# Performance work log

Hardware: AMD Instinct MI355X
Metric: run time of the kernel (lower is better)

The kernel has to match this reference:

```python
import jax, jax.numpy as jnp
import numpy as np

NF, NH1, NH21, NH22, NCLS = 6, 128, 128, 128, 3
OBS_X, OBS_Y, OBS_Z, R = 10.0, 10.0, 9.0, 7.0
BATCH = 131072


def setup_inputs() -> dict:
    key = jax.random.key(0)
    ks = jax.random.split(key, 16)
    def lin(kw, kb, fan_in, fan_out):
        bound = 1.0 / np.sqrt(fan_in)
        w = jax.random.uniform(kw, (fan_out, fan_in), jnp.float32, -bound, bound)
        b = jax.random.uniform(kb, (fan_out,), jnp.float32, -bound, bound)
        return w, b
    fc1_w, fc1_b = lin(ks[0], ks[1], NF, NH1)
    fc21_w, fc21_b = lin(ks[2], ks[3], NH1, NH21)
    fc22_w, fc22_b = lin(ks[4], ks[5], NH1, NH22)
    fcm1_w, fcm1_b = lin(ks[6], ks[7], NH21, NH21)
    fcm2_w, fcm2_b = lin(ks[8], ks[9], NH22, NH22)
    fc31_w, fc31_b = lin(ks[10], ks[11], NH21, NCLS)
    fc32_w, fc32_b = lin(ks[12], ks[13], NH22, 2)
    x = jax.random.normal(ks[14], (BATCH, NF), jnp.float32)
    mean = jnp.array([10.0, 0.0, 10.0, 0.0, 9.0, 0.0], jnp.float32)
    std = jnp.array([5.0, 2.0, 5.0, 2.0, 5.0, 2.0], jnp.float32)
    return {"x": x, "mean": mean, "std": std,
            "fc1_w": fc1_w, "fc1_b": fc1_b,
            "fc21_w": fc21_w, "fc21_b": fc21_b,
            "fc22_w": fc22_w, "fc22_b": fc22_b,
            "fcm1_w": fcm1_w, "fcm1_b": fcm1_b,
            "fcm2_w": fcm2_w, "fcm2_b": fcm2_b,
            "fc31_w": fc31_w, "fc31_b": fc31_b,
            "fc32_w": fc32_w, "fc32_b": fc32_b,
            "sgn": 1}


def _forward(x, mean, std, fc1_w, fc1_b, fc21_w, fc21_b, fc22_w, fc22_b,
             fcm1_w, fcm1_b, fcm2_w, fcm2_b, fc31_w, fc31_b, fc32_w, fc32_b):
    x0 = x * std + mean                                   # de-normalized state [B,6]
    h = jnp.tanh(x @ fc1_w.T + fc1_b)                     # [B,NH1]
    x21 = jnp.tanh(h @ fc21_w.T + fc21_b)
    x22 = jnp.tanh(h @ fc22_w.T + fc22_b)
    x21 = jnp.tanh(x21 @ fcm1_w.T + fcm1_b)
    x22 = jnp.tanh(x22 @ fcm2_w.T + fcm2_b)
    x31 = x21 @ fc31_w.T + fc31_b                         # QP linear term p, [B,3]
    x32 = 4.0 * jax.nn.sigmoid(x22 @ fc32_w.T + fc32_b)   # HOCBF penalties, [B,2]

    # higher-order CBF terms
    px, vx, py, vy, pz, vz = (x0[:, i] for i in range(6))
    dx, dy, dz = px - OBS_X, py - OBS_Y, pz - OBS_Z
    barrier = dx**4 + dy**4 + dz**4 - R**4
    barrier_dot = 4.0 * (dx**3 * vx + dy**3 * vy + dz**3 * vz)
    Lf2b = 12.0 * (dx**2 * vx**2 + dy**2 * vy**2 + dz**2 * vz**2)
    G = -4.0 * jnp.stack([dx**3, dy**3, dz**3], axis=-1)  # [B,3], single constraint G u <= h
    hvec = Lf2b + (x32[:, 0] + x32[:, 1]) * barrier_dot + x32[:, 0] * x32[:, 1] * barrier  # [B]

    # QP: min 0.5 u^T u + x31^T u  s.t.  G u <= h  (Q = I, one constraint)
    # Closed-form KKT: u = -x31 - lam*G, lam = max(0, (G @ (-x31) - h) / (G @ G))
    u_unc = -x31
    Gu = jnp.sum(G * u_unc, axis=-1)                      # [B]
    GG = jnp.sum(G * G, axis=-1)                          # [B]
    lam = jnp.maximum(Gu - hvec, 0.0) / GG
    u = u_unc - lam[:, None] * G                          # [B,3]
    return u


def reference(x, mean, std, fc1_w, fc1_b, fc21_w, fc21_b, fc22_w, fc22_b,
              fcm1_w, fcm1_b, fcm2_w, fcm2_b, fc31_w, fc31_b, fc32_w, fc32_b, sgn):
    return _forward(x, mean, std, fc1_w, fc1_b, fc21_w, fc21_b, fc22_w, fc22_b,
                    fcm1_w, fcm1_b, fcm2_w, fcm2_b, fc31_w, fc31_b, fc32_w, fc32_b)
```

## Files before the change

### kernel.cpp

```cpp
#include <hip/hip_runtime.h>

typedef _Float16 half8 __attribute__((ext_vector_type(8)));
typedef _Float16 half4_t __attribute__((ext_vector_type(4)));
typedef float float4_t __attribute__((ext_vector_type(4)));

#define SB 32
#define NT 256

#define OFF_W1   0
#define OFF_W21  4096
#define OFF_W22  20480
#define OFF_WM1  36864
#define OFF_WM2  53248
#define OFF_W4   69632
#define OFF_BIAS 70272
#define WS_WELEMS 70272

__device__ __forceinline__ float fast_tanh(float x) {
  float e = __builtin_amdgcn_exp2f(x * 2.8853900817779268f);
  return fmaf(-2.f, __builtin_amdgcn_rcpf(1.f + e), 1.f);
}
__device__ __forceinline__ float sigmoid4(float z) {
  float e = __builtin_amdgcn_exp2f(-z * 1.4426950408889634f);
  return 4.f * __builtin_amdgcn_rcpf(1.f + e);
}

__global__ void prepack(const float* __restrict__ w1, const float* __restrict__ w21,
                        const float* __restrict__ w22, const float* __restrict__ wm1,
                        const float* __restrict__ wm2, const float* __restrict__ w31,
                        const float* __restrict__ w32, const float* __restrict__ b1,
                        const float* __restrict__ b21, const float* __restrict__ b22,
                        const float* __restrict__ bm1, const float* __restrict__ bm2,
                        _Float16* __restrict__ ws) {
  const int stride = gridDim.x * blockDim.x;
  for (int i = blockIdx.x * blockDim.x + threadIdx.x; i < WS_WELEMS; i += stride) {
    float v;
    if (i < OFF_W21) {
      int t = i;
      int j = t & 7, c = t >> 3, l16 = c & 15, t1 = c >> 4;
      int k8 = t1 & 3, mt = t1 >> 2;
      int row = mt * 16 + l16, k = k8 * 8 + j;
      v = (k < 6) ? w1[row * 6 + k] : 0.f;
    } else if (i < OFF_W4) {
      int t = i - OFF_W21;
      int m = t >> 14; t &= 16383;
      const float* src = (m == 0) ? w21 : (m == 1) ? w22 : (m == 2) ? wm1 : wm2;
      int j = t & 7, c = t >> 3, l16 = c & 15, t1 = c >> 4;
      int k8 = t1 & 15, mt = t1 >> 4;
      v = src[(mt * 16 + l16) * 128 + k8 * 8 + j];
    } else {
      int t = i - OFF_W4;
      int r = t >> 7, k = t & 127;
      v = (r < 3) ? w31[r * 128 + k] : w32[(r - 3) * 128 + k];
    }
    ws[i] = (_Float16)v;
  }
  float* bws = (float*)(ws + OFF_BIAS);
  for (int i = blockIdx.x * blockDim.x + threadIdx.x; i < 640; i += stride) {
    int layer = i >> 7, idx = i & 127;
    const float* src = (layer == 0) ? b1 : (layer == 1) ? b21
                     : (layer == 2) ? b22 : (layer == 3) ? bm1 : bm2;
    bws[i] = src[idx];
  }
}

template <int K, int SBX>
__device__ __forceinline__ void gemm_layer(const _Float16* __restrict__ Wg,
                                           const _Float16* __restrict__ inB,
                                           const float* __restrict__ biasG,
                                           _Float16* __restrict__ outB) {
  constexpr int KC = K / 8;
  constexpr int KS = K / 32;
  constexpr int NTT = SBX / 16;
  constexpr int RS = SBX * 8;
  const int tid  = threadIdx.x;
  const int wv   = tid >> 6;
  const int lane = tid & 63;
  const int quad = lane >> 4;
  const int l16  = lane & 15;
  const int mt0 = wv * 2, mt1 = mt0 + 1;

  half8 a0[KS], a1[KS];
#pragma unroll
  for (int kk = 0; kk < KS; ++kk) {
    a0[kk] = *(const half8*)(Wg + ((mt0 * KC + kk * 4 + quad) * 16 + l16) * 8);
    a1[kk] = *(const half8*)(Wg + ((mt1 * KC + kk * 4 + quad) * 16 + l16) * 8);
  }
  float4_t acc0[NTT], acc1[NTT];
#pragma unroll
  for (int nt = 0; nt < NTT; ++nt) {
    acc0[nt] = (float4_t){0.f, 0.f, 0.f, 0.f};
    acc1[nt] = (float4_t){0.f, 0.f, 0.f, 0.f};
  }
#pragma unroll
  for (int kk = 0; kk < KS; ++kk) {
#pragma unroll
    for (int nt = 0; nt < NTT; ++nt) {
      half8 b = *(const half8*)(inB + (kk * 4 + quad) * RS + (nt * 16 + l16) * 8);
      acc0[nt] = __builtin_amdgcn_mfma_f32_16x16x32_f16(a0[kk], b, acc0[nt], 0, 0, 0);
      acc1[nt] = __builtin_amdgcn_mfma_f32_16x16x32_f16(a1[kk], b, acc1[nt], 0, 0, 0);
    }
  }
  const float4_t bv0 = *(const float4_t*)(biasG + mt0 * 16 + quad * 4);
  const float4_t bv1 = *(const float4_t*)(biasG + mt1 * 16 + quad * 4);
  const int ob0 = mt0 * 16 + quad * 4;
  const int ob1 = mt1 * 16 + quad * 4;
#pragma unroll
  for (int nt = 0; nt < NTT; ++nt) {
    const int s = nt * 16 + l16;
    half4_t h0, h1;
#pragma unroll
    for (int r = 0; r < 4; ++r) {
      h0[r] = (_Float16)fast_tanh(acc0[nt][r] + bv0[r]);
      h1[r] = (_Float16)fast_tanh(acc1[nt][r] + bv1[r]);
    }
    *(half4_t*)(outB + (ob0 >> 3) * RS + s * 8 + (ob0 & 7)) = h0;
    *(half4_t*)(outB + (ob1 >> 3) * RS + s * 8 + (ob1 & 7)) = h1;
  }
}

__global__ __launch_bounds__(NT, 5) void bnet_main(
    const float* __restrict__ x, const float* __restrict__ meang,
    const float* __restrict__ stdg, const float* __restrict__ b31,
    const float* __restrict__ b32, const _Float16* __restrict__ ws,
    float* __restrict__ out) {
  __shared__ __align__(16) _Float16 bufH[SB * 128];
  __shared__ __align__(16) _Float16 bufA[SB * 128];
  __shared__ __align__(16) _Float16 bufB[SB * 128];
  __shared__ __align__(16) unsigned char uni[NT * 5 * 4];

  _Float16* xb = (_Float16*)uni;
  float* part = (float*)uni;

  const int tid = threadIdx.x;
  const int s0 = blockIdx.x * SB;
  const float* biasW = (const float*)(ws + OFF_BIAS);

  if (tid < 128) {
    const int s = tid & 31, k8 = tid >> 5;
    half8 v;
#pragma unroll
    for (int j = 0; j < 8; ++j) v[j] = (_Float16)0.f;
    if (k8 == 0) {
      const float* xp = x + (size_t)(s0 + s) * 6;
#pragma unroll
      for (int j = 0; j < 6; ++j) v[j] = (_Float16)xp[j];
    }
    *(half8*)(xb + k8 * (SB * 8) + s * 8) = v;
  }
  __syncthreads();

  gemm_layer<32, SB>(ws + OFF_W1, xb, biasW, bufH);
  __syncthreads();
  gemm_layer<128, SB>(ws + OFF_W21, bufH, biasW + 128, bufA);
  gemm_layer<128, SB>(ws + OFF_W22, bufH, biasW + 256, bufB);
  __syncthreads();
  gemm_layer<128, SB>(ws + OFF_WM1, bufA, biasW + 384, bufH);
  __syncthreads();
  gemm_layer<128, SB>(ws + OFF_WM2, bufB, biasW + 512, bufA);
  __syncthreads();

  {
    const int s = tid & 31, q = tid >> 5;
    half8 xm1a = *(const half8*)(bufH + (2 * q + 0) * (SB * 8) + s * 8);
    half8 xm1b = *(const half8*)(bufH + (2 * q + 1) * (SB * 8) + s * 8);
    half8 xm2a = *(const half8*)(bufA + (2 * q + 0) * (SB * 8) + s * 8);
    half8 xm2b = *(const half8*)(bufA + (2 * q + 1) * (SB * 8) + s * 8);
    float res[5];
#pragma unroll
    for (int j = 0; j < 5; ++j) {
      const _Float16* wr = ws + OFF_W4 + j * 128 + q * 16;
      half8 wa = *(const half8*)(wr);
      half8 wb = *(const half8*)(wr + 8);
      half8 xa = (j < 3) ? xm1a : xm2a;
      half8 xc = (j < 3) ? xm1b : xm2b;
      float acc = 0.f;
#pragma unroll
      for (int e = 0; e < 8; ++e) acc = fmaf((float)xa[e], (float)wa[e], acc);
#pragma unroll
      for (int e = 0; e < 8; ++e) acc = fmaf((float)xc[e], (float)wb[e], acc);
      res[j] = acc;
    }
    __syncthreads();
#pragma unroll
    for (int j = 0; j < 5; ++j) part[tid * 5 + j] = res[j];
  }
  __syncthreads();

  if (tid < SB) {
    const int s = tid;
    float r[5];
#pragma unroll
    for (int j = 0; j < 5; ++j) {
      float a = 0.f;
#pragma unroll
      for (int q = 0; q < 8; ++q) a += part[(q * 32 + s) * 5 + j];
      r[j] = a;
    }
    float u0 = -(r[0] + b31[0]);
    float u1 = -(r[1] + b31[1]);
    float u2 = -(r[2] + b31[2]);
    float p0 = sigmoid4(r[3] + b32[0]);
    float p1 = sigmoid4(r[4] + b32[1]);
    const float* xp = x + (size_t)(s0 + s) * 6;
    float px = xp[0] * stdg[0] + meang[0];
    float vx = xp[1] * stdg[1] + meang[1];
    float py = xp[2] * stdg[2] + meang[2];
    float vy = xp[3] * stdg[3] + meang[3];
    float pz = xp[4] * stdg[4] + meang[4];
    float vz = xp[5] * stdg[5] + meang[5];
    float dx = px - 10.f, dy = py - 10.f, dz = pz - 9.f;
    float dx2 = dx * dx, dy2 = dy * dy, dz2 = dz * dz;
    float dx3 = dx2 * dx, dy3 = dy2 * dy, dz3 = dz2 * dz;
    float barrier = dx3 * dx + dy3 * dy + dz3 * dz - 2401.f;
    float bdot = 4.f * (dx3 * vx + dy3 * vy + dz3 * vz);
    float Lf2b = 12.f * (dx2 * vx * vx + dy2 * vy * vy + dz2 * vz * vz);
    float g0 = -4.f * dx3, g1 = -4.f * dy3, g2 = -4.f * dz3;
    float hv = Lf2b + (p0 + p1) * bdot + p0 * p1 * barrier;
    float Gu = g0 * u0 + g1 * u1 + g2 * u2;
    float GG = g0 * g0 + g1 * g1 + g2 * g2;
    float lam = fmaxf(Gu - hv, 0.f) / GG;
    float* op = out + (size_t)(s0 + s) * 3;
    op[0] = u0 - lam * g0;
    op[1] = u1 - lam * g1;
    op[2] = u2 - lam * g2;
  }
}

extern "C" void kernel_launch(void* const* d_in, const int* in_sizes, int n_in,
                              void* d_out, int out_size, void* d_ws, size_t ws_size,
                              hipStream_t stream) {
  const float* x    = (const float*)d_in[0];
  const float* mean = (const float*)d_in[1];
  const float* stdv = (const float*)d_in[2];
  const float* w1   = (const float*)d_in[3];
  const float* b1   = (const float*)d_in[4];
  const float* w21  = (const float*)d_in[5];
  const float* b21  = (const float*)d_in[6];
  const float* w22  = (const float*)d_in[7];
  const float* b22  = (const float*)d_in[8];
  const float* wm1  = (const float*)d_in[9];
  const float* bm1  = (const float*)d_in[10];
  const float* wm2  = (const float*)d_in[11];
  const float* bm2  = (const float*)d_in[12];
  const float* w31  = (const float*)d_in[13];
  const float* b31  = (const float*)d_in[14];
  const float* w32  = (const float*)d_in[15];
  const float* b32  = (const float*)d_in[16];
  _Float16* ws = (_Float16*)d_ws;
  float* out = (float*)d_out;
  const int batch = in_sizes[0] / 6;

  hipLaunchKernelGGL(prepack, dim3(96), dim3(NT), 0, stream,
                     w1, w21, w22, wm1, wm2, w31, w32,
                     b1, b21, b22, bm1, bm2, ws);
  hipLaunchKernelGGL(bnet_main, dim3(batch / SB), dim3(NT), 0, stream,
                     x, mean, stdv, b31, b32, (const _Float16*)ws, out);
}
```

Measured before the change: 134.8 us.

## Keep all layer weights in registers and loop over multiple batch tiles per block

Drops the separate prepack kernel. Each block now loads the fp32 weights once, converts them to fp16 MFMA fragments, keeps them in registers, and processes 8 batch tiles in a loop, prefetching the next tile's inputs. The goal is to remove the per-tile global weight reloads and one kernel launch. In exchange, register pressure rises sharply, so launch bounds drop to 2 blocks per CU and the grid shrinks to 512 blocks. Lower occupancy could reduce latency hiding.

```diff
diff --git a/kernel.cpp b/kernel.cpp
--- a/kernel.cpp
+++ b/kernel.cpp
@@ -6,15 +6,8 @@
 
 #define SB 32
 #define NT 256
-
-#define OFF_W1   0
-#define OFF_W21  4096
-#define OFF_W22  20480
-#define OFF_WM1  36864
-#define OFF_WM2  53248
-#define OFF_W4   69632
-#define OFF_BIAS 70272
-#define WS_WELEMS 70272
+#define TPB 8
+#define RS (SB * 8)
 
 __device__ __forceinline__ float fast_tanh(float x) {
   float e = __builtin_amdgcn_exp2f(x * 2.8853900817779268f);
@@ -24,206 +17,218 @@
   float e = __builtin_amdgcn_exp2f(-z * 1.4426950408889634f);
   return 4.f * __builtin_amdgcn_rcpf(1.f + e);
 }
-
-__global__ void prepack(const float* __restrict__ w1, const float* __restrict__ w21,
-                        const float* __restrict__ w22, const float* __restrict__ wm1,
-                        const float* __restrict__ wm2, const float* __restrict__ w31,
-                        const float* __restrict__ w32, const float* __restrict__ b1,
-                        const float* __restrict__ b21, const float* __restrict__ b22,
-                        const float* __restrict__ bm1, const float* __restrict__ bm2,
-                        _Float16* __restrict__ ws) {
-  const int stride = gridDim.x * blockDim.x;
-  for (int i = blockIdx.x * blockDim.x + threadIdx.x; i < WS_WELEMS; i += stride) {
-    float v;
-    if (i < OFF_W21) {
-      int t = i;
-      int j = t & 7, c = t >> 3, l16 = c & 15, t1 = c >> 4;
-      int k8 = t1 & 3, mt = t1 >> 2;
-      int row = mt * 16 + l16, k = k8 * 8 + j;
-      v = (k < 6) ? w1[row * 6 + k] : 0.f;
-    } else if (i < OFF_W4) {
-      int t = i - OFF_W21;
-      int m = t >> 14; t &= 16383;
-      const float* src = (m == 0) ? w21 : (m == 1) ? w22 : (m == 2) ? wm1 : wm2;
-      int j = t & 7, c = t >> 3, l16 = c & 15, t1 = c >> 4;
-      int k8 = t1 & 15, mt = t1 >> 4;
-      v = src[(mt * 16 + l16) * 128 + k8 * 8 + j];
-    } else {
-      int t = i - OFF_W4;
-      int r = t >> 7, k = t & 127;
-      v = (r < 3) ? w31[r * 128 + k] : w32[(r - 3) * 128 + k];
-    }
-    ws[i] = (_Float16)v;
-  }
-  float* bws = (float*)(ws + OFF_BIAS);
-  for (int i = blockIdx.x * blockDim.x + threadIdx.x; i < 640; i += stride) {
+__device__ __forceinline__ half8 pack8(float4_t lo, float4_t hi) {
+  half8 r;
+#pragma unroll
+  for (int j = 0; j < 4; ++j) { r[j] = (_Float16)lo[j]; r[j + 4] = (_Float16)hi[j]; }
+  return r;
+}
+
+template <int KS>
+__device__ __forceinline__ void gemm_r(const half8* __restrict__ a0,
+                                       const half8* __restrict__ a1,
+                                       const _Float16* __restrict__ inB,
+                                       const float* __restrict__ biasL,
+                                       _Float16* __restrict__ outB,
+                                       int quad, int l16, int mt0, int mt1) {
+  float4_t acc0[2], acc1[2];
+#pragma unroll
+  for (int nt = 0; nt < 2; ++nt) {
+    acc0[nt] = (float4_t){0.f, 0.f, 0.f, 0.f};
+    acc1[nt] = (float4_t){0.f, 0.f, 0.f, 0.f};
+  }
+#pragma unroll
+  for (int kk = 0; kk < KS; ++kk) {
+#pragma unroll
+    for (int nt = 0; nt < 2; ++nt) {
+      half8 b = *(const half8*)(inB + (kk * 4 + quad) * RS + (nt * 16 + l16) * 8);
+      acc0[nt] = __builtin_amdgcn_mfma_f32_16x16x32_f16(a0[kk], b, acc0[nt], 0, 0, 0);
+      acc1[nt] = __builtin_amdgcn_mfma_f32_16x16x32_f16(a1[kk], b, acc1[nt], 0, 0, 0);
+    }
+  }
+  const float4_t bv0 = *(const float4_t*)(biasL + mt0 * 16 + quad * 4);
+  const float4_t bv1 = *(const float4_t*)(biasL + mt1 * 16 + quad * 4);
+  const int ob0 = mt0 * 16 + quad * 4;
+  const int ob1 = mt1 * 16 + quad * 4;
+#pragma unroll
+  for (int nt = 0; nt < 2; ++nt) {
+    const int s = nt * 16 + l16;
+    half4_t h0, h1;
+#pragma unroll
+    for (int r = 0; r < 4; ++r) {
+      h0[r] = (_Float16)fast_tanh(acc0[nt][r] + bv0[r]);
+      h1[r] = (_Float16)fast_tanh(acc1[nt][r] + bv1[r]);
+    }
+    *(half4_t*)(outB + (ob0 >> 3) * RS + s * 8 + (ob0 & 7)) = h0;
+    *(half4_t*)(outB + (ob1 >> 3) * RS + s * 8 + (ob1 & 7)) = h1;
+  }
+}
+
+__global__ __launch_bounds__(NT, 2) void bnet_main(
+    const float* __restrict__ x, const float* __restrict__ meang,
+    const float* __restrict__ stdg, const float* __restrict__ w1,
+    const float* __restrict__ b1, const float* __restrict__ w21,
+    const float* __restrict__ b21, const float* __restrict__ w22,
+    const float* __restrict__ b22, const float* __restrict__ wm1,
+    const float* __restrict__ bm1, const float* __restrict__ wm2,
+    const float* __restrict__ bm2, const float* __restrict__ w31,
+    const float* __restrict__ b31, const float* __restrict__ w32,
+    const float* __restrict__ b32, float* __restrict__ out, int ntiles) {
+  __shared__ __align__(16) _Float16 xb[SB * 32];
+  __shared__ __align__(16) _Float16 bufH[SB * 128];
+  __shared__ __align__(16) _Float16 bufA[SB * 128];
+  __shared__ __align__(16) _Float16 bufB[SB * 128];
+  __shared__ __align__(16) _Float16 bufC[SB * 128];
+  __shared__ __align__(16) float bias_l[5 * 128];
+  __shared__ __align__(16) _Float16 w4l[5 * 128];
+  __shared__ float b345[5];
+  __shared__ __align__(16) float part[NT * 5];
+
+  const int tid = threadIdx.x;
+  const int wv = tid >> 6;
+  const int lane = tid & 63;
+  const int quad = lane >> 4;
+  const int l16 = lane & 15;
+  const int mt0 = wv * 2, mt1 = mt0 + 1;
+
+  for (int i = tid; i < 640; i += NT) {
     int layer = i >> 7, idx = i & 127;
     const float* src = (layer == 0) ? b1 : (layer == 1) ? b21
                      : (layer == 2) ? b22 : (layer == 3) ? bm1 : bm2;
-    bws[i] = src[idx];
-  }
-}
-
-template <int K, int SBX>
-__device__ __forceinline__ void gemm_layer(const _Float16* __restrict__ Wg,
-                                           const _Float16* __restrict__ inB,
-                                           const float* __restrict__ biasG,
-                                           _Float16* __restrict__ outB) {
-  constexpr int KC = K / 8;
-  constexpr int KS = K / 32;
-  constexpr int NTT = SBX / 16;
-  constexpr int RS = SBX * 8;
-  const int tid  = threadIdx.x;
-  const int wv   = tid >> 6;
-  const int lane = tid & 63;
-  const int quad = lane >> 4;
-  const int l16  = lane & 15;
-  const int mt0 = wv * 2, mt1 = mt0 + 1;
-
-  half8 a0[KS], a1[KS];
-#pragma unroll
-  for (int kk = 0; kk < KS; ++kk) {
-    a0[kk] = *(const half8*)(Wg + ((mt0 * KC + kk * 4 + quad) * 16 + l16) * 8);
-    a1[kk] = *(const half8*)(Wg + ((mt1 * KC + kk * 4 + quad) * 16 + l16) * 8);
-  }
-  float4_t acc0[NTT], acc1[NTT];
-#pragma unroll
-  for (int nt = 0; nt < NTT; ++nt) {
-    acc0[nt] = (float4_t){0.f, 0.f, 0.f, 0.f};
-    acc1[nt] = (float4_t){0.f, 0.f, 0.f, 0.f};
-  }
-#pragma unroll
-  for (int kk = 0; kk < KS; ++kk) {
-#pragma unroll
-    for (int nt = 0; nt < NTT; ++nt) {
-      half8 b = *(const half8*)(inB + (kk * 4 + quad) * RS + (nt * 16 + l16) * 8);
-      acc0[nt] = __builtin_amdgcn_mfma_f32_16x16x32_f16(a0[kk], b, acc0[nt], 0, 0, 0);
-      acc1[nt] = __builtin_amdgcn_mfma_f32_16x16x32_f16(a1[kk], b, acc1[nt], 0, 0, 0);
-    }
-  }
-  const float4_t bv0 = *(const float4_t*)(biasG + mt0 * 16 + quad * 4);
-  const float4_t bv1 = *(const float4_t*)(biasG + mt1 * 16 + quad * 4);
-  const int ob0 = mt0 * 16 + quad * 4;
-  const int ob1 = mt1 * 16 + quad * 4;
-#pragma unroll
-  for (int nt = 0; nt < NTT; ++nt) {
-    const int s = nt * 16 + l16;
-    half4_t h0, h1;
-#pragma unroll
-    for (int r = 0; r < 4; ++r) {
-      h0[r] = (_Float16)fast_tanh(acc0[nt][r] + bv0[r]);
-      h1[r] = (_Float16)fast_tanh(acc1[nt][r] + bv1[r]);
-    }
-    *(half4_t*)(outB + (ob0 >> 3) * RS + s * 8 + (ob0 & 7)) = h0;
-    *(half4_t*)(outB + (ob1 >> 3) * RS + s * 8 + (ob1 & 7)) = h1;
-  }
-}
-
-__global__ __launch_bounds__(NT, 5) void bnet_main(
-    const float* __restrict__ x, const float* __restrict__ meang,
-    const float* __restrict__ stdg, const float* __restrict__ b31,
-    const float* __restrict__ b32, const _Float16* __restrict__ ws,
-    float* __restrict__ out) {
-  __shared__ __align__(16) _Float16 bufH[SB * 128];
-  __shared__ __align__(16) _Float16 bufA[SB * 128];
-  __shared__ __align__(16) _Float16 bufB[SB * 128];
-  __shared__ __align__(16) unsigned char uni[NT * 5 * 4];
-
-  _Float16* xb = (_Float16*)uni;
-  float* part = (float*)uni;
-
-  const int tid = threadIdx.x;
-  const int s0 = blockIdx.x * SB;
-  const float* biasW = (const float*)(ws + OFF_BIAS);
-
-  if (tid < 128) {
-    const int s = tid & 31, k8 = tid >> 5;
+    bias_l[i] = src[idx];
+    int r = i >> 7, k = i & 127;
+    w4l[i] = (_Float16)((r < 3) ? w31[r * 128 + k] : w32[(r - 3) * 128 + k]);
+  }
+  if (tid < 5) b345[tid] = (tid < 3) ? b31[tid] : b32[tid - 3];
+  if (tid < 96) {
+    half8 z;
+#pragma unroll
+    for (int j = 0; j < 8; ++j) z[j] = (_Float16)0.f;
+    *(half8*)(xb + ((tid >> 5) + 1) * RS + (tid & 31) * 8) = z;
+  }
+
+  half8 A1[2];
+  half8 A21[2][4], A22[2][4], AM1[2][4], AM2[2][4];
+#pragma unroll
+  for (int m = 0; m < 2; ++m) {
+    const int row = (mt0 + m) * 16 + l16;
     half8 v;
 #pragma unroll
     for (int j = 0; j < 8; ++j) v[j] = (_Float16)0.f;
-    if (k8 == 0) {
-      const float* xp = x + (size_t)(s0 + s) * 6;
-#pragma unroll
-      for (int j = 0; j < 6; ++j) v[j] = (_Float16)xp[j];
-    }
-    *(half8*)(xb + k8 * (SB * 8) + s * 8) = v;
-  }
-  __syncthreads();
-
-  gemm_layer<32, SB>(ws + OFF_W1, xb, biasW, bufH);
-  __syncthreads();
-  gemm_layer<128, SB>(ws + OFF_W21, bufH, biasW + 128, bufA);
-  gemm_layer<128, SB>(ws + OFF_W22, bufH, biasW + 256, bufB);
-  __syncthreads();
-  gemm_layer<128, SB>(ws + OFF_WM1, bufA, biasW + 384, bufH);
-  __syncthreads();
-  gemm_layer<128, SB>(ws + OFF_WM2, bufB, biasW + 512, bufA);
-  __syncthreads();
-
-  {
-    const int s = tid & 31, q = tid >> 5;
-    half8 xm1a = *(const half8*)(bufH + (2 * q + 0) * (SB * 8) + s * 8);
-    half8 xm1b = *(const half8*)(bufH + (2 * q + 1) * (SB * 8) + s * 8);
-    half8 xm2a = *(const half8*)(bufA + (2 * q + 0) * (SB * 8) + s * 8);
-    half8 xm2b = *(const half8*)(bufA + (2 * q + 1) * (SB * 8) + s * 8);
-    float res[5];
-#pragma unroll
-    for (int j = 0; j < 5; ++j) {
-      const _Float16* wr = ws + OFF_W4 + j * 128 + q * 16;
-      half8 wa = *(const half8*)(wr);
-      half8 wb = *(const half8*)(wr + 8);
-      half8 xa = (j < 3) ? xm1a : xm2a;
-      half8 xc = (j < 3) ? xm1b : xm2b;
-      float acc = 0.f;
-#pragma unroll
-      for (int e = 0; e < 8; ++e) acc = fmaf((float)xa[e], (float)wa[e], acc);
-#pragma unroll
-      for (int e = 0; e < 8; ++e) acc = fmaf((float)xc[e], (float)wb[e], acc);
-      res[j] = acc;
-    }
-    __syncthreads();
-#pragma unroll
-    for (int j = 0; j < 5; ++j) part[tid * 5 + j] = res[j];
-  }
-  __syncthreads();
-
+    if (quad == 0) {
+#pragma unroll
+      for (int j = 0; j < 6; ++j) v[j] = (_Float16)w1[row * 6 + j];
+    }
+    A1[m] = v;
+#pragma unroll
+    for (int kk = 0; kk < 4; ++kk) {
+      const int base = row * 128 + kk * 32 + quad * 8;
+      A21[m][kk] = pack8(*(const float4_t*)(w21 + base), *(const float4_t*)(w21 + base + 4));
+      A22[m][kk] = pack8(*(const float4_t*)(w22 + base), *(const float4_t*)(w22 + base + 4));
+      AM1[m][kk] = pack8(*(const float4_t*)(wm1 + base), *(const float4_t*)(wm1 + base + 4));
+      AM2[m][kk] = pack8(*(const float4_t*)(wm2 + base), *(const float4_t*)(wm2 + base + 4));
+    }
+  }
+
+  const int tile0 = blockIdx.x * TPB;
+  float xr[6];
   if (tid < SB) {
-    const int s = tid;
-    float r[5];
-#pragma unroll
-    for (int j = 0; j < 5; ++j) {
-      float a = 0.f;
-#pragma unroll
-      for (int q = 0; q < 8; ++q) a += part[(q * 32 + s) * 5 + j];
-      r[j] = a;
-    }
-    float u0 = -(r[0] + b31[0]);
-    float u1 = -(r[1] + b31[1]);
-    float u2 = -(r[2] + b31[2]);
-    float p0 = sigmoid4(r[3] + b32[0]);
-    float p1 = sigmoid4(r[4] + b32[1]);
-    const float* xp = x + (size_t)(s0 + s) * 6;
-    float px = xp[0] * stdg[0] + meang[0];
-    float vx = xp[1] * stdg[1] + meang[1];
-    float py = xp[2] * stdg[2] + meang[2];
-    float vy = xp[3] * stdg[3] + meang[3];
-    float pz = xp[4] * stdg[4] + meang[4];
-    float vz = xp[5] * stdg[5] + meang[5];
-    float dx = px - 10.f, dy = py - 10.f, dz = pz - 9.f;
-    float dx2 = dx * dx, dy2 = dy * dy, dz2 = dz * dz;
-    float dx3 = dx2 * dx, dy3 = dy2 * dy, dz3 = dz2 * dz;
-    float barrier = dx3 * dx + dy3 * dy + dz3 * dz - 2401.f;
-    float bdot = 4.f * (dx3 * vx + dy3 * vy + dz3 * vz);
-    float Lf2b = 12.f * (dx2 * vx * vx + dy2 * vy * vy + dz2 * vz * vz);
-    float g0 = -4.f * dx3, g1 = -4.f * dy3, g2 = -4.f * dz3;
-    float hv = Lf2b + (p0 + p1) * bdot + p0 * p1 * barrier;
-    float Gu = g0 * u0 + g1 * u1 + g2 * u2;
-    float GG = g0 * g0 + g1 * g1 + g2 * g2;
-    float lam = fmaxf(Gu - hv, 0.f) / GG;
-    float* op = out + (size_t)(s0 + s) * 3;
-    op[0] = u0 - lam * g0;
-    op[1] = u1 - lam * g1;
-    op[2] = u2 - lam * g2;
+    const int tc = (tile0 < ntiles) ? tile0 : (ntiles - 1);
+    const float* xp = x + ((size_t)tc * SB + tid) * 6;
+#pragma unroll
+    for (int j = 0; j < 6; ++j) xr[j] = xp[j];
+  }
+
+  for (int t = 0; t < TPB; ++t) {
+    const int tile = tile0 + t;
+    if (tile >= ntiles) break;
+    float xc[6];
+    if (tid < SB) {
+      half8 v;
+#pragma unroll
+      for (int j = 0; j < 6; ++j) { v[j] = (_Float16)xr[j]; xc[j] = xr[j]; }
+      v[6] = (_Float16)0.f; v[7] = (_Float16)0.f;
+      *(half8*)(xb + tid * 8) = v;
+      const int tn = (tile + 1 < ntiles) ? (tile + 1) : (ntiles - 1);
+      const float* xp = x + ((size_t)tn * SB + tid) * 6;
+#pragma unroll
+      for (int j = 0; j < 6; ++j) xr[j] = xp[j];
+    }
+    __syncthreads();
+
+    gemm_r<1>(&A1[0], &A1[1], xb, bias_l, bufH, quad, l16, mt0, mt1);
+    __syncthreads();
+    gemm_r<4>(A21[0], A21[1], bufH, bias_l + 128, bufA, quad, l16, mt0, mt1);
+    gemm_r<4>(A22[0], A22[1], bufH, bias_l + 256, bufB, quad, l16, mt0, mt1);
+    __syncthreads();
+    gemm_r<4>(AM1[0], AM1[1], bufA, bias_l + 384, bufH, quad, l16, mt0, mt1);
+    gemm_r<4>(AM2[0], AM2[1], bufB, bias_l + 512, bufC, quad, l16, mt0, mt1);
+    __syncthreads();
+
+    {
+      const int s = tid & 31, q = tid >> 5;
+      half8 x1a = *(const half8*)(bufH + (2 * q + 0) * RS + s * 8);
+      half8 x1b = *(const half8*)(bufH + (2 * q + 1) * RS + s * 8);
+      half8 x2a = *(const half8*)(bufC + (2 * q + 0) * RS + s * 8);
+      half8 x2b = *(const half8*)(bufC + (2 * q + 1) * RS + s * 8);
+      float res[5];
+#pragma unroll
+      for (int j = 0; j < 5; ++j) {
+        const _Float16* wr = w4l + j * 128 + q * 16;
+        half8 wa = *(const half8*)(wr);
+        half8 wb = *(const half8*)(wr + 8);
+        half8 xa = (j < 3) ? x1a : x2a;
+        half8 xcv = (j < 3) ? x1b : x2b;
+        float acc = 0.f;
+#pragma unroll
+        for (int e = 0; e < 8; ++e) acc = fmaf((float)xa[e], (float)wa[e], acc);
+#pragma unroll
+        for (int e = 0; e < 8; ++e) acc = fmaf((float)xcv[e], (float)wb[e], acc);
+        res[j] = acc;
+      }
+#pragma unroll
+      for (int j = 0; j < 5; ++j) part[tid * 5 + j] = res[j];
+    }
+    __syncthreads();
+
+    if (tid < SB) {
+      const int s = tid;
+      float r[5];
+#pragma unroll
+      for (int j = 0; j < 5; ++j) {
+        float a = 0.f;
+#pragma unroll
+        for (int q = 0; q < 8; ++q) a += part[(q * 32 + s) * 5 + j];
+        r[j] = a;
+      }
+      float u0 = -(r[0] + b345[0]);
+      float u1 = -(r[1] + b345[1]);
+      float u2 = -(r[2] + b345[2]);
+      float p0 = sigmoid4(r[3] + b345[3]);
+      float p1 = sigmoid4(r[4] + b345[4]);
+      float px = xc[0] * stdg[0] + meang[0];
+      float vx = xc[1] * stdg[1] + meang[1];
+      float py = xc[2] * stdg[2] + meang[2];
+      float vy = xc[3] * stdg[3] + meang[3];
+      float pz = xc[4] * stdg[4] + meang[4];
+      float vz = xc[5] * stdg[5] + meang[5];
+      float dx = px - 10.f, dy = py - 10.f, dz = pz - 9.f;
+      float dx2 = dx * dx, dy2 = dy * dy, dz2 = dz * dz;
+      float dx3 = dx2 * dx, dy3 = dy2 * dy, dz3 = dz2 * dz;
+      float barrier = dx3 * dx + dy3 * dy + dz3 * dz - 2401.f;
+      float bdot = 4.f * (dx3 * vx + dy3 * vy + dz3 * vz);
+      float Lf2b = 12.f * (dx2 * vx * vx + dy2 * vy * vy + dz2 * vz * vz);
+      float g0 = -4.f * dx3, g1 = -4.f * dy3, g2 = -4.f * dz3;
+      float hv = Lf2b + (p0 + p1) * bdot + p0 * p1 * barrier;
+      float Gu = g0 * u0 + g1 * u1 + g2 * u2;
+      float GG = g0 * g0 + g1 * g1 + g2 * g2;
+      float lam = fmaxf(Gu - hv, 0.f) / GG;
+      float* op = out + ((size_t)tile * SB + s) * 3;
+      op[0] = u0 - lam * g0;
+      op[1] = u1 - lam * g1;
+      op[2] = u2 - lam * g2;
+    }
+    __syncthreads();
   }
 }
 
@@ -247,13 +252,12 @@
   const float* b31  = (const float*)d_in[14];
   const float* w32  = (const float*)d_in[15];
   const float* b32  = (const float*)d_in[16];
-  _Float16* ws = (_Float16*)d_ws;
   float* out = (float*)d_out;
   const int batch = in_sizes[0] / 6;
-
-  hipLaunchKernelGGL(prepack, dim3(96), dim3(NT), 0, stream,
-                     w1, w21, w22, wm1, wm2, w31, w32,
-                     b1, b21, b22, bm1, bm2, ws);
-  hipLaunchKernelGGL(bnet_main, dim3(batch / SB), dim3(NT), 0, stream,
-                     x, mean, stdv, b31, b32, (const _Float16*)ws, out);
-}
+  const int ntiles = batch / SB;
+  const int nblk = (ntiles + TPB - 1) / TPB;
+
+  hipLaunchKernelGGL(bnet_main, dim3(nblk), dim3(NT), 0, stream,
+                     x, mean, stdv, w1, b1, w21, b21, w22, b22,
+                     wm1, bm1, wm2, bm2, w31, b31, w32, b32, out, ntiles);
+}
```

Result: slower. 148.8 us (+10.4%).

## Run head layers on MFMA and feed first layer directly from registers

Applied to the files above, without the earlier changes.

The final 128-to-5 head projections move from per-thread scalar FMA dot products with a shared-memory partial-sum reduction onto MFMA, using zero-padded 16-row weight tiles that a single wavefront runs over both chains. The input layer now builds its B fragments straight from global memory in registers, which drops the input staging buffer and one barrier. Launch bounds go from 5 to 6 blocks per CU now that the shared scratch area is gone. The cost is mostly wasted MFMA rows on the padded head tiles, plus the QP epilogue running on only 16 lanes of a single wavefront.

```diff
diff --git a/kernel.cpp b/kernel.cpp
--- a/kernel.cpp
+++ b/kernel.cpp
@@ -3,18 +3,20 @@
 typedef _Float16 half8 __attribute__((ext_vector_type(8)));
 typedef _Float16 half4_t __attribute__((ext_vector_type(4)));
 typedef float float4_t __attribute__((ext_vector_type(4)));
+typedef float float2_t __attribute__((ext_vector_type(2)));
 
 #define SB 32
 #define NT 256
+#define RS (SB * 8)
 
 #define OFF_W1   0
 #define OFF_W21  4096
 #define OFF_W22  20480
 #define OFF_WM1  36864
 #define OFF_WM2  53248
-#define OFF_W4   69632
-#define OFF_BIAS 70272
-#define WS_WELEMS 70272
+#define OFF_W4A  69632
+#define OFF_BIAS 73728
+#define WS_HELEMS 73728
 
 __device__ __forceinline__ float fast_tanh(float x) {
   float e = __builtin_amdgcn_exp2f(x * 2.8853900817779268f);
@@ -33,7 +35,7 @@
                         const float* __restrict__ bm1, const float* __restrict__ bm2,
                         _Float16* __restrict__ ws) {
   const int stride = gridDim.x * blockDim.x;
-  for (int i = blockIdx.x * blockDim.x + threadIdx.x; i < WS_WELEMS; i += stride) {
+  for (int i = blockIdx.x * blockDim.x + threadIdx.x; i < WS_HELEMS; i += stride) {
     float v;
     if (i < OFF_W21) {
       int t = i;
@@ -41,7 +43,7 @@
       int k8 = t1 & 3, mt = t1 >> 2;
       int row = mt * 16 + l16, k = k8 * 8 + j;
       v = (k < 6) ? w1[row * 6 + k] : 0.f;
-    } else if (i < OFF_W4) {
+    } else if (i < OFF_W4A) {
       int t = i - OFF_W21;
       int m = t >> 14; t &= 16383;
       const float* src = (m == 0) ? w21 : (m == 1) ? w22 : (m == 2) ? wm1 : wm2;
@@ -49,9 +51,12 @@
       int k8 = t1 & 15, mt = t1 >> 4;
       v = src[(mt * 16 + l16) * 128 + k8 * 8 + j];
     } else {
-      int t = i - OFF_W4;
-      int r = t >> 7, k = t & 127;
-      v = (r < 3) ? w31[r * 128 + k] : w32[(r - 3) * 128 + k];
+      int t = i - OFF_W4A;
+      int j = t & 7, r = t >> 3, l16 = r & 15, q = r >> 4;
+      int cc = q & 15, chain = q >> 4;
+      int k = cc * 8 + j, m = l16;
+      if (chain == 0) v = (m < 3) ? w31[m * 128 + k] : 0.f;
+      else            v = (m < 2) ? w32[m * 128 + k] : 0.f;
     }
     ws[i] = (_Float16)v;
   }
@@ -64,49 +69,38 @@
   }
 }
 
-template <int K, int SBX>
-__device__ __forceinline__ void gemm_layer(const _Float16* __restrict__ Wg,
-                                           const _Float16* __restrict__ inB,
-                                           const float* __restrict__ biasG,
-                                           _Float16* __restrict__ outB) {
-  constexpr int KC = K / 8;
-  constexpr int KS = K / 32;
-  constexpr int NTT = SBX / 16;
-  constexpr int RS = SBX * 8;
-  const int tid  = threadIdx.x;
-  const int wv   = tid >> 6;
-  const int lane = tid & 63;
-  const int quad = lane >> 4;
-  const int l16  = lane & 15;
-  const int mt0 = wv * 2, mt1 = mt0 + 1;
-
-  half8 a0[KS], a1[KS];
-#pragma unroll
-  for (int kk = 0; kk < KS; ++kk) {
-    a0[kk] = *(const half8*)(Wg + ((mt0 * KC + kk * 4 + quad) * 16 + l16) * 8);
-    a1[kk] = *(const half8*)(Wg + ((mt1 * KC + kk * 4 + quad) * 16 + l16) * 8);
-  }
-  float4_t acc0[NTT], acc1[NTT];
-#pragma unroll
-  for (int nt = 0; nt < NTT; ++nt) {
+__device__ __forceinline__ void gemm128(const _Float16* __restrict__ Wg,
+                                        const float* __restrict__ biasG,
+                                        const _Float16* __restrict__ inB,
+                                        _Float16* __restrict__ outB,
+                                        int quad, int l16, int mt0, int mt1) {
+  const float4_t bv0 = *(const float4_t*)(biasG + mt0 * 16 + quad * 4);
+  const float4_t bv1 = *(const float4_t*)(biasG + mt1 * 16 + quad * 4);
+  half8 a0[4], a1[4];
+#pragma unroll
+  for (int kk = 0; kk < 4; ++kk) {
+    a0[kk] = *(const half8*)(Wg + ((mt0 * 16 + kk * 4 + quad) * 16 + l16) * 8);
+    a1[kk] = *(const half8*)(Wg + ((mt1 * 16 + kk * 4 + quad) * 16 + l16) * 8);
+  }
+  float4_t acc0[2], acc1[2];
+#pragma unroll
+  for (int nt = 0; nt < 2; ++nt) {
     acc0[nt] = (float4_t){0.f, 0.f, 0.f, 0.f};
     acc1[nt] = (float4_t){0.f, 0.f, 0.f, 0.f};
   }
 #pragma unroll
-  for (int kk = 0; kk < KS; ++kk) {
-#pragma unroll
-    for (int nt = 0; nt < NTT; ++nt) {
+  for (int kk = 0; kk < 4; ++kk) {
+#pragma unroll
+    for (int nt = 0; nt < 2; ++nt) {
       half8 b = *(const half8*)(inB + (kk * 4 + quad) * RS + (nt * 16 + l16) * 8);
       acc0[nt] = __builtin_amdgcn_mfma_f32_16x16x32_f16(a0[kk], b, acc0[nt], 0, 0, 0);
       acc1[nt] = __builtin_amdgcn_mfma_f32_16x16x32_f16(a1[kk], b, acc1[nt], 0, 0, 0);
     }
   }
-  const float4_t bv0 = *(const float4_t*)(biasG + mt0 * 16 + quad * 4);
-  const float4_t bv1 = *(const float4_t*)(biasG + mt1 * 16 + quad * 4);
   const int ob0 = mt0 * 16 + quad * 4;
   const int ob1 = mt1 * 16 + quad * 4;
 #pragma unroll
-  for (int nt = 0; nt < NTT; ++nt) {
+  for (int nt = 0; nt < 2; ++nt) {
     const int s = nt * 16 + l16;
     half4_t h0, h1;
 #pragma unroll
@@ -119,7 +113,7 @@
   }
 }
 
-__global__ __launch_bounds__(NT, 5) void bnet_main(
+__global__ __launch_bounds__(NT, 6) void bnet_main(
     const float* __restrict__ x, const float* __restrict__ meang,
     const float* __restrict__ stdg, const float* __restrict__ b31,
     const float* __restrict__ b32, const _Float16* __restrict__ ws,
@@ -127,103 +121,132 @@
   __shared__ __align__(16) _Float16 bufH[SB * 128];
   __shared__ __align__(16) _Float16 bufA[SB * 128];
   __shared__ __align__(16) _Float16 bufB[SB * 128];
-  __shared__ __align__(16) unsigned char uni[NT * 5 * 4];
-
-  _Float16* xb = (_Float16*)uni;
-  float* part = (float*)uni;
 
   const int tid = threadIdx.x;
+  const int wv = tid >> 6;
+  const int lane = tid & 63;
+  const int quad = lane >> 4;
+  const int l16 = lane & 15;
+  const int mt0 = wv * 2, mt1 = mt0 + 1;
   const int s0 = blockIdx.x * SB;
-  const float* biasW = (const float*)(ws + OFF_BIAS);
-
-  if (tid < 128) {
-    const int s = tid & 31, k8 = tid >> 5;
-    half8 v;
-#pragma unroll
-    for (int j = 0; j < 8; ++j) v[j] = (_Float16)0.f;
-    if (k8 == 0) {
-      const float* xp = x + (size_t)(s0 + s) * 6;
-#pragma unroll
-      for (int j = 0; j < 6; ++j) v[j] = (_Float16)xp[j];
-    }
-    *(half8*)(xb + k8 * (SB * 8) + s * 8) = v;
-  }
-  __syncthreads();
-
-  gemm_layer<32, SB>(ws + OFF_W1, xb, biasW, bufH);
-  __syncthreads();
-  gemm_layer<128, SB>(ws + OFF_W21, bufH, biasW + 128, bufA);
-  gemm_layer<128, SB>(ws + OFF_W22, bufH, biasW + 256, bufB);
-  __syncthreads();
-  gemm_layer<128, SB>(ws + OFF_WM1, bufA, biasW + 384, bufH);
-  __syncthreads();
-  gemm_layer<128, SB>(ws + OFF_WM2, bufB, biasW + 512, bufA);
-  __syncthreads();
+  const float* biasF = (const float*)(ws + OFF_BIAS);
 
   {
-    const int s = tid & 31, q = tid >> 5;
-    half8 xm1a = *(const half8*)(bufH + (2 * q + 0) * (SB * 8) + s * 8);
-    half8 xm1b = *(const half8*)(bufH + (2 * q + 1) * (SB * 8) + s * 8);
-    half8 xm2a = *(const half8*)(bufA + (2 * q + 0) * (SB * 8) + s * 8);
-    half8 xm2b = *(const half8*)(bufA + (2 * q + 1) * (SB * 8) + s * 8);
-    float res[5];
-#pragma unroll
-    for (int j = 0; j < 5; ++j) {
-      const _Float16* wr = ws + OFF_W4 + j * 128 + q * 16;
-      half8 wa = *(const half8*)(wr);
-      half8 wb = *(const half8*)(wr + 8);
-      half8 xa = (j < 3) ? xm1a : xm2a;
-      half8 xc = (j < 3) ? xm1b : xm2b;
-      float acc = 0.f;
-#pragma unroll
-      for (int e = 0; e < 8; ++e) acc = fmaf((float)xa[e], (float)wa[e], acc);
-#pragma unroll
-      for (int e = 0; e < 8; ++e) acc = fmaf((float)xc[e], (float)wb[e], acc);
-      res[j] = acc;
-    }
-    __syncthreads();
-#pragma unroll
-    for (int j = 0; j < 5; ++j) part[tid * 5 + j] = res[j];
-  }
-  __syncthreads();
-
-  if (tid < SB) {
-    const int s = tid;
-    float r[5];
-#pragma unroll
-    for (int j = 0; j < 5; ++j) {
-      float a = 0.f;
-#pragma unroll
-      for (int q = 0; q < 8; ++q) a += part[(q * 32 + s) * 5 + j];
-      r[j] = a;
-    }
-    float u0 = -(r[0] + b31[0]);
-    float u1 = -(r[1] + b31[1]);
-    float u2 = -(r[2] + b31[2]);
-    float p0 = sigmoid4(r[3] + b32[0]);
-    float p1 = sigmoid4(r[4] + b32[1]);
-    const float* xp = x + (size_t)(s0 + s) * 6;
-    float px = xp[0] * stdg[0] + meang[0];
-    float vx = xp[1] * stdg[1] + meang[1];
-    float py = xp[2] * stdg[2] + meang[2];
-    float vy = xp[3] * stdg[3] + meang[3];
-    float pz = xp[4] * stdg[4] + meang[4];
-    float vz = xp[5] * stdg[5] + meang[5];
-    float dx = px - 10.f, dy = py - 10.f, dz = pz - 9.f;
-    float dx2 = dx * dx, dy2 = dy * dy, dz2 = dz * dz;
-    float dx3 = dx2 * dx, dy3 = dy2 * dy, dz3 = dz2 * dz;
-    float barrier = dx3 * dx + dy3 * dy + dz3 * dz - 2401.f;
-    float bdot = 4.f * (dx3 * vx + dy3 * vy + dz3 * vz);
-    float Lf2b = 12.f * (dx2 * vx * vx + dy2 * vy * vy + dz2 * vz * vz);
-    float g0 = -4.f * dx3, g1 = -4.f * dy3, g2 = -4.f * dz3;
-    float hv = Lf2b + (p0 + p1) * bdot + p0 * p1 * barrier;
-    float Gu = g0 * u0 + g1 * u1 + g2 * u2;
-    float GG = g0 * g0 + g1 * g1 + g2 * g2;
-    float lam = fmaxf(Gu - hv, 0.f) / GG;
-    float* op = out + (size_t)(s0 + s) * 3;
-    op[0] = u0 - lam * g0;
-    op[1] = u1 - lam * g1;
-    op[2] = u2 - lam * g2;
+    half8 bx[2];
+#pragma unroll
+    for (int nt = 0; nt < 2; ++nt) {
+      half8 v;
+#pragma unroll
+      for (int j = 0; j < 8; ++j) v[j] = (_Float16)0.f;
+      if (quad == 0) {
+        const float* xp = x + (size_t)(s0 + nt * 16 + l16) * 6;
+        float2_t e0 = *(const float2_t*)(xp);
+        float2_t e1 = *(const float2_t*)(xp + 2);
+        float2_t e2 = *(const float2_t*)(xp + 4);
+        v[0] = (_Float16)e0[0]; v[1] = (_Float16)e0[1];
+        v[2] = (_Float16)e1[0]; v[3] = (_Float16)e1[1];
+        v[4] = (_Float16)e2[0]; v[5] = (_Float16)e2[1];
+      }
+      bx[nt] = v;
+    }
+    const float4_t bv0 = *(const float4_t*)(biasF + mt0 * 16 + quad * 4);
+    const float4_t bv1 = *(const float4_t*)(biasF + mt1 * 16 + quad * 4);
+    half8 a0 = *(const half8*)(ws + OFF_W1 + ((mt0 * 4 + quad) * 16 + l16) * 8);
+    half8 a1 = *(const half8*)(ws + OFF_W1 + ((mt1 * 4 + quad) * 16 + l16) * 8);
+    float4_t acc0[2], acc1[2];
+#pragma unroll
+    for (int nt = 0; nt < 2; ++nt) {
+      acc0[nt] = (float4_t){0.f, 0.f, 0.f, 0.f};
+      acc1[nt] = (float4_t){0.f, 0.f, 0.f, 0.f};
+      acc0[nt] = __builtin_amdgcn_mfma_f32_16x16x32_f16(a0, bx[nt], acc0[nt], 0, 0, 0);
+      acc1[nt] = __builtin_amdgcn_mfma_f32_16x16x32_f16(a1, bx[nt], acc1[nt], 0, 0, 0);
+    }
+    const int ob0 = mt0 * 16 + quad * 4;
+    const int ob1 = mt1 * 16 + quad * 4;
+#pragma unroll
+    for (int nt = 0; nt < 2; ++nt) {
+      const int s = nt * 16 + l16;
+      half4_t h0, h1;
+#pragma unroll
+      for (int r = 0; r < 4; ++r) {
+        h0[r] = (_Float16)fast_tanh(acc0[nt][r] + bv0[r]);
+        h1[r] = (_Float16)fast_tanh(acc1[nt][r] + bv1[r]);
+      }
+      *(half4_t*)(bufH + (ob0 >> 3) * RS + s * 8 + (ob0 & 7)) = h0;
+      *(half4_t*)(bufH + (ob1 >> 3) * RS + s * 8 + (ob1 & 7)) = h1;
+    }
+  }
+  __syncthreads();
+
+  gemm128(ws + OFF_W21, biasF + 128, bufH, bufA, quad, l16, mt0, mt1);
+  gemm128(ws + OFF_W22, biasF + 256, bufH, bufB, quad, l16, mt0, mt1);
+  __syncthreads();
+  gemm128(ws + OFF_WM1, biasF + 384, bufA, bufH, quad, l16, mt0, mt1);
+  __syncthreads();
+  gemm128(ws + OFF_WM2, biasF + 512, bufB, bufA, quad, l16, mt0, mt1);
+  __syncthreads();
+
+  if (wv == 0) {
+    half8 a4[2][4];
+#pragma unroll
+    for (int c = 0; c < 2; ++c)
+#pragma unroll
+      for (int kk = 0; kk < 4; ++kk)
+        a4[c][kk] = *(const half8*)(ws + OFF_W4A +
+                                    ((c * 16 + kk * 4 + quad) * 16 + l16) * 8);
+    float4_t acc[2][2];
+#pragma unroll
+    for (int c = 0; c < 2; ++c)
+#pragma unroll
+      for (int nt = 0; nt < 2; ++nt) acc[c][nt] = (float4_t){0.f, 0.f, 0.f, 0.f};
+#pragma unroll
+    for (int kk = 0; kk < 4; ++kk)
+#pragma unroll
+      for (int nt = 0; nt < 2; ++nt) {
+        half8 b1f = *(const half8*)(bufH + (kk * 4 + quad) * RS + (nt * 16 + l16) * 8);
+        half8 b2f = *(const half8*)(bufA + (kk * 4 + quad) * RS + (nt * 16 + l16) * 8);
+        acc[0][nt] = __builtin_amdgcn_mfma_f32_16x16x32_f16(a4[0][kk], b1f, acc[0][nt], 0, 0, 0);
+        acc[1][nt] = __builtin_amdgcn_mfma_f32_16x16x32_f16(a4[1][kk], b2f, acc[1][nt], 0, 0, 0);
+      }
+    if (quad == 0) {
+      const float m0 = meang[0], m1 = meang[1], m2 = meang[2];
+      const float m3 = meang[3], m4 = meang[4], m5 = meang[5];
+      const float sd0 = stdg[0], sd1 = stdg[1], sd2 = stdg[2];
+      const float sd3 = stdg[3], sd4 = stdg[4], sd5 = stdg[5];
+      const float c31_0 = b31[0], c31_1 = b31[1], c31_2 = b31[2];
+      const float c32_0 = b32[0], c32_1 = b32[1];
+#pragma unroll
+      for (int nt = 0; nt < 2; ++nt) {
+        const int s = nt * 16 + l16;
+        float u0 = -(acc[0][nt][0] + c31_0);
+        float u1 = -(acc[0][nt][1] + c31_1);
+        float u2 = -(acc[0][nt][2] + c31_2);
+        float p0 = sigmoid4(acc[1][nt][0] + c32_0);
+        float p1 = sigmoid4(acc[1][nt][1] + c32_1);
+        const float* xp = x + (size_t)(s0 + s) * 6;
+        float2_t e0 = *(const float2_t*)(xp);
+        float2_t e1 = *(const float2_t*)(xp + 2);
+        float2_t e2 = *(const float2_t*)(xp + 4);
+        float px = e0[0] * sd0 + m0, vx = e0[1] * sd1 + m1;
+        float py = e1[0] * sd2 + m2, vy = e1[1] * sd3 + m3;
+        float pz = e2[0] * sd4 + m4, vz = e2[1] * sd5 + m5;
+        float dx = px - 10.f, dy = py - 10.f, dz = pz - 9.f;
+        float dx2 = dx * dx, dy2 = dy * dy, dz2 = dz * dz;
+        float dx3 = dx2 * dx, dy3 = dy2 * dy, dz3 = dz2 * dz;
+        float barrier = dx3 * dx + dy3 * dy + dz3 * dz - 2401.f;
+        float bdot = 4.f * (dx3 * vx + dy3 * vy + dz3 * vz);
+        float Lf2b = 12.f * (dx2 * vx * vx + dy2 * vy * vy + dz2 * vz * vz);
+        float g0 = -4.f * dx3, g1 = -4.f * dy3, g2 = -4.f * dz3;
+        float hv = Lf2b + (p0 + p1) * bdot + p0 * p1 * barrier;
+        float Gu = g0 * u0 + g1 * u1 + g2 * u2;
+        float GG = g0 * g0 + g1 * g1 + g2 * g2;
+        float lam = fmaxf(Gu - hv, 0.f) / GG;
+        float* op = out + (size_t)(s0 + s) * 3;
+        op[0] = u0 - lam * g0;
+        op[1] = u1 - lam * g1;
+        op[2] = u2 - lam * g2;
+      }
+    }
   }
 }
 
```

Result: no change. 133.4 us (-1.1%).
